# Optimization experiments

Hardware: AMD Instinct MI355X
Metric: run time of the kernel (lower is better)

Reference implementation:

```python
import jax, jax.numpy as jnp
import numpy as np

HID, HQ, HKV, D, W = 2880, 64, 8, 64, 128  # hidden, q heads, kv heads, head_dim, sliding window
SCALE = D ** -0.5
NEG = -1e30


def _rope(x, cos, sin):
    # x: [B,S,H,D]; cos/sin: [S, D//2]
    c = cos[None, :, None, :].astype(x.dtype)
    s = sin[None, :, None, :].astype(x.dtype)
    x1, x2 = jnp.split(x, 2, axis=-1)
    return jnp.concatenate([x1 * c - x2 * s, x2 * c + x1 * s], axis=-1)


def setup_inputs() -> dict:
    key = jax.random.key(0)
    ks = jax.random.split(key, 12)
    B, S = 1, 4096
    std = 0.02
    x = jax.random.normal(ks[0], (B, S, HID), jnp.float32)
    # realistic rotary table (cos || sin), half-dim each
    inv_freq = 1.0 / (150000.0 ** (np.arange(0, D, 2, dtype=np.float32) / D))
    ang = np.arange(S, dtype=np.float32)[:, None] * inv_freq[None, :]
    freqs_cis = jnp.asarray(np.concatenate([np.cos(ang), np.sin(ang)], axis=-1), jnp.float32)  # [S, D]
    Wq = jax.random.normal(ks[1], (HID, HQ * D), jnp.float32) * std
    bq = jnp.zeros((HQ * D,), jnp.float32)
    Wk = jax.random.normal(ks[2], (HID, HKV * D), jnp.float32) * std
    bk = jnp.zeros((HKV * D,), jnp.float32)
    Wv = jax.random.normal(ks[3], (HID, HKV * D), jnp.float32) * std
    bv = jnp.zeros((HKV * D,), jnp.float32)
    Wo = jax.random.normal(ks[4], (HQ * D, HID), jnp.float32) * std
    bo = jnp.zeros((HID,), jnp.float32)
    sinks = jax.random.normal(ks[5], (HQ,), jnp.float32) * std
    return {"x": x, "freqs_cis": freqs_cis, "Wq": Wq, "bq": bq, "Wk": Wk, "bk": bk,
            "Wv": Wv, "bv": bv, "Wo": Wo, "bo": bo, "sinks": sinks}


def reference(x, freqs_cis, Wq, bq, Wk, bk, Wv, bv, Wo, bo, sinks):
    B, S, _ = x.shape
    G = HQ // HKV
    nb = S // W  # S must be a multiple of W
    cos, sin = jnp.split(freqs_cis, 2, axis=-1)

    q = (x @ Wq + bq).reshape(B, S, HQ, D)
    k = (x @ Wk + bk).reshape(B, S, HKV, D)
    v = (x @ Wv + bv).reshape(B, S, HKV, D)
    q = _rope(q, cos, sin)
    k = _rope(k, cos, sin)

    q = q.transpose(0, 2, 1, 3)  # [B,HQ,S,D]
    k = k.transpose(0, 2, 1, 3)  # [B,HKV,S,D]
    v = v.transpose(0, 2, 1, 3)

    # blocked sliding-window: each query block of size W sees keys [blk*W - W, blk*W + W)
    qb = q.reshape(B, HKV, G, nb, W, D)
    kp = jnp.pad(k, ((0, 0), (0, 0), (W, 0), (0, 0)))  # prepend W zero keys
    vp = jnp.pad(v, ((0, 0), (0, 0), (W, 0), (0, 0)))
    widx = jnp.arange(nb)[:, None] * W + jnp.arange(2 * W)[None, :]  # [nb, 2W]
    kb = kp[:, :, widx]  # [B,HKV,nb,2W,D]
    vb = vp[:, :, widx]

    scores = jnp.einsum('bkgntd,bkncd->bkgntc', qb, kb) * SCALE  # [B,HKV,G,nb,W,2W]

    t = jnp.arange(W)[:, None]
    j = jnp.arange(2 * W)[None, :]
    band = (j >= t + 1) & (j <= t + W)  # 0 <= qpos - kpos <= W-1
    kpos_ok = (jnp.arange(nb)[:, None] * W - W + jnp.arange(2 * W)[None, :]) >= 0  # [nb,2W]
    mask = band[None, :, :] & kpos_ok[:, None, :]  # [nb,W,2W]
    scores = jnp.where(mask[None, None, None], scores, NEG)

    sink = sinks.reshape(HKV, G)[None, :, :, None, None]  # [1,HKV,G,1,1]
    m = jnp.maximum(scores.max(axis=-1), sink)  # [B,HKV,G,nb,W]
    e = jnp.exp(scores - m[..., None])
    denom = e.sum(axis=-1) + jnp.exp(sink - m)
    p = e / denom[..., None]

    o = jnp.einsum('bkgntc,bkncd->bkgntd', p, vb)  # [B,HKV,G,nb,W,D]
    o = o.reshape(B, HQ, S, D).transpose(0, 2, 1, 3).reshape(B, S, HQ * D)
    return o @ Wo + bo
```

## Files before the change

kernel.cpp:

```cpp
#include <hip/hip_runtime.h>
#include <hip/hip_bf16.h>
#include <stdint.h>


typedef __attribute__((ext_vector_type(8))) short bf16x8;
typedef __attribute__((ext_vector_type(4))) float f32x4;
typedef __attribute__((ext_vector_type(8))) unsigned short ushort8;

#define DEVI static __device__ __forceinline__

DEVI unsigned short f2bf(float f) {
  unsigned x = __float_as_uint(f);
  return (unsigned short)((x + 0x7fffu + ((x >> 16) & 1u)) >> 16);
}
DEVI float bf2f(unsigned short u) { return __uint_as_float(((unsigned)u) << 16); }

DEVI void async16(const void* g, void* l) {
  __builtin_amdgcn_global_load_lds(
      (const __attribute__((address_space(1))) void*)g,
      (__attribute__((address_space(3))) void*)l, 16, 0, 0);
}

__global__ void k_cast_bf16(const float* __restrict__ src,
                            unsigned short* __restrict__ dst, long n) {
  long i = ((long)blockIdx.x * blockDim.x + threadIdx.x) * 4;
  const long stride = (long)gridDim.x * blockDim.x * 4;
  for (; i < n; i += stride) {
    float4 v = *(const float4*)(src + i);
    ushort4 o = make_ushort4(f2bf(v.x), f2bf(v.y), f2bf(v.z), f2bf(v.w));
    *(ushort4*)(dst + i) = o;
  }
}

__global__ void k_transpose_cast(const float* __restrict__ src,
                                 unsigned short* __restrict__ dst,
                                 int R, int C) {
  __shared__ float tile[64][65];
  const int t = threadIdx.x;
  const int r0 = blockIdx.y * 64, c0 = blockIdx.x * 64;
#pragma unroll
  for (int i = 0; i < 16; i++) {
    int r = i * 4 + (t >> 6), c = t & 63;
    float v = 0.f;
    if (c0 + c < C) v = src[(long)(r0 + r) * C + c0 + c];
    tile[r][c] = v;
  }
  __syncthreads();
#pragma unroll
  for (int i = 0; i < 16; i++) {
    int nn = i * 4 + (t >> 6), kk = t & 63;
    dst[(long)(c0 + nn) * R + r0 + kk] = f2bf(tile[kk][nn]);
  }
}

__global__ void k_concat_bias(const float* __restrict__ bq,
                              const float* __restrict__ bk,
                              const float* __restrict__ bv,
                              float* __restrict__ dst) {
  int i = blockIdx.x * 256 + threadIdx.x;
  if (i < 5120)
    dst[i] = (i < 4096) ? bq[i] : ((i < 4608) ? bk[i - 4096] : bv[i - 4608]);
}

template <bool OUT_BF16, bool NMASK>
__global__ __launch_bounds__(256) void k_gemm_bt(
    const unsigned short* __restrict__ A, const unsigned short* __restrict__ Bt,
    const float* __restrict__ bias, void* __restrict__ Cout, int M, int K,
    int ldc, int Nreal) {
  __shared__ unsigned short As[128 * 32];
  __shared__ unsigned short Bs[128 * 32];
  const int tid = threadIdx.x;
  const int w = tid >> 6, l = tid & 63;
  const int wm = w >> 1, wn = w & 1;
  const int lg = l >> 4, ll = l & 15;
  const long m0 = (long)blockIdx.x * 128;
  const long n0 = (long)blockIdx.y * 128;

  f32x4 acc[4][4];
#pragma unroll
  for (int i = 0; i < 4; i++)
#pragma unroll
    for (int j = 0; j < 4; j++) acc[i][j] = (f32x4){0.f, 0.f, 0.f, 0.f};

  const unsigned short* ga = A + (m0 + 32 * w + (l >> 2)) * (long)K + (l & 3) * 8;
  const unsigned short* gb = Bt + (n0 + 32 * w + (l >> 2)) * (long)K + (l & 3) * 8;
  unsigned short* lA = As + 32 * w * 32;
  unsigned short* lB = Bs + 32 * w * 32;

  for (int kt = 0; kt < K; kt += 32) {
    async16(ga + kt, lA);
    async16(ga + kt + 16 * (long)K, lA + 16 * 32);
    async16(gb + kt, lB);
    async16(gb + kt + 16 * (long)K, lB + 16 * 32);
    __syncthreads();
    bf16x8 af[4], bfr[4];
#pragma unroll
    for (int m = 0; m < 4; m++)
      af[m] = *(const bf16x8*)&As[(wm * 64 + m * 16 + ll) * 32 + 8 * lg];
#pragma unroll
    for (int nn = 0; nn < 4; nn++)
      bfr[nn] = *(const bf16x8*)&Bs[(wn * 64 + nn * 16 + ll) * 32 + 8 * lg];
#pragma unroll
    for (int m = 0; m < 4; m++)
#pragma unroll
      for (int nn = 0; nn < 4; nn++)
        acc[m][nn] = __builtin_amdgcn_mfma_f32_16x16x32_bf16(af[m], bfr[nn],
                                                             acc[m][nn], 0, 0, 0);
    __syncthreads();
  }

#pragma unroll
  for (int nn = 0; nn < 4; nn++) {
    int col = (int)n0 + wn * 64 + nn * 16 + ll;
    bool ok = (!NMASK) || (col < Nreal);
    float bv_ = ok ? bias[col] : 0.f;
#pragma unroll
    for (int m = 0; m < 4; m++) {
      long row = m0 + wm * 64 + m * 16 + lg * 4;
#pragma unroll
      for (int j = 0; j < 4; j++) {
        float v = acc[m][nn][j] + bv_;
        if (ok) {
          if (OUT_BF16)
            ((unsigned short*)Cout)[(row + j) * (long)ldc + col] = f2bf(v);
          else
            ((float*)Cout)[(row + j) * (long)ldc + col] = v;
        }
      }
    }
  }
}

__global__ void k_rope(unsigned short* __restrict__ qkv,
                       const float* __restrict__ fc) {
  const int s = blockIdx.x;
  const float* f = fc + (long)s * 64;
  unsigned short* row = qkv + (long)s * 5120;
  for (int i = threadIdx.x; i < 72 * 32; i += 256) {
    int hh = i >> 5, d = i & 31;
    float c = f[d], sn = f[32 + d];
    int base = hh * 64 + d;
    float x1 = bf2f(row[base]), x2 = bf2f(row[base + 32]);
    row[base] = f2bf(x1 * c - x2 * sn);
    row[base + 32] = f2bf(x2 * c + x1 * sn);
  }
}

__global__ void k_transpose_v(const unsigned short* __restrict__ qkv,
                              unsigned short* __restrict__ vt) {
  __shared__ unsigned short tile[64][72];
  const int t = threadIdx.x;
  const int ts = blockIdx.x;
  const int tj = blockIdx.y;
#pragma unroll
  for (int i = 0; i < 2; i++) {
    int s = i * 32 + (t >> 3), j = (t & 7) * 8;
    *(ushort8*)&tile[s][j] =
        *(const ushort8*)(qkv + (long)(ts * 64 + s) * 5120 + 4608 + tj * 64 + j);
  }
  __syncthreads();
  int j = t >> 2, s0 = (t & 3) * 16;
  ushort8 v0, v1;
#pragma unroll
  for (int x = 0; x < 8; x++) {
    v0[x] = tile[s0 + x][j];
    v1[x] = tile[s0 + 8 + x][j];
  }
  unsigned short* dst = vt + (long)(tj * 64 + j) * 4096 + ts * 64 + s0;
  *(ushort8*)dst = v0;
  *(ushort8*)(dst + 8) = v1;
}

__global__ __launch_bounds__(256) void k_attn(
    const unsigned short* __restrict__ qkv, const unsigned short* __restrict__ vt,
    const float* __restrict__ sinks, unsigned short* __restrict__ o) {
  __shared__ unsigned short Ps[4][32][136];
  __shared__ unsigned short Ks[128][72];
  __shared__ unsigned short Vts[64][136];
  unsigned short(*Qs)[72] = (unsigned short(*)[72]) & Ps[0][0][0];

  const int n = blockIdx.x, h = blockIdx.y;
  const int kvh = h >> 3;
  const int t = threadIdx.x, w = t >> 6, l = t & 63;
  const int lg = l >> 4, ll = l & 15;

#pragma unroll
  for (int i = 0; i < 4; i++) {
    int s = 32 * i + (t >> 3), c8 = (t & 7) * 8;
    *(ushort8*)&Qs[s][c8] =
        *(const ushort8*)(qkv + (long)(n * 128 + s) * 5120 + h * 64 + c8);
  }
  __syncthreads();
  bf16x8 aq[2][2];
#pragma unroll
  for (int m = 0; m < 2; m++)
#pragma unroll
    for (int ks = 0; ks < 2; ks++)
      aq[m][ks] = *(const bf16x8*)&Qs[32 * w + 16 * m + ll][32 * ks + 8 * lg];

  f32x4 oacc[2][4];
#pragma unroll
  for (int m = 0; m < 2; m++)
#pragma unroll
    for (int nt = 0; nt < 4; nt++) oacc[m][nt] = (f32x4){0.f, 0.f, 0.f, 0.f};
  float mrun[2][4], lrun[2][4];
#pragma unroll
  for (int m = 0; m < 2; m++)
#pragma unroll
    for (int j = 0; j < 4; j++) { mrun[m][j] = -3.0e38f; lrun[m][j] = 0.f; }

  for (int ch = (n == 0 ? 1 : 0); ch < 2; ch++) {
    const int kbase = (n - 1 + ch) * 128;
#pragma unroll
    for (int i = 0; i < 4; i++) {
      int c = 32 * i + (t >> 3), c8 = (t & 7) * 8;
      *(ushort8*)&Ks[c][c8] = *(const ushort8*)(
          qkv + (long)(kbase + c) * 5120 + 4096 + kvh * 64 + c8);
    }
#pragma unroll
    for (int i = 0; i < 4; i++) {
      int d = 16 * i + (t >> 4), c8 = (t & 15) * 8;
      *(ushort8*)&Vts[d][c8] =
          *(const ushort8*)(vt + (long)(kvh * 64 + d) * 4096 + kbase + c8);
    }
    __syncthreads();

    f32x4 sacc[2][8];
#pragma unroll
    for (int m = 0; m < 2; m++)
#pragma unroll
      for (int ct = 0; ct < 8; ct++) sacc[m][ct] = (f32x4){0.f, 0.f, 0.f, 0.f};
#pragma unroll
    for (int ct = 0; ct < 8; ct++)
#pragma unroll
      for (int ks = 0; ks < 2; ks++) {
        bf16x8 bk = *(const bf16x8*)&Ks[16 * ct + ll][32 * ks + 8 * lg];
#pragma unroll
        for (int m = 0; m < 2; m++)
          sacc[m][ct] =
              __builtin_amdgcn_mfma_f32_16x16x32_bf16(aq[m][ks], bk, sacc[m][ct], 0, 0, 0);
      }

    float cmax[2][4];
#pragma unroll
    for (int m = 0; m < 2; m++)
#pragma unroll
      for (int j = 0; j < 4; j++) cmax[m][j] = -3.0e38f;
#pragma unroll
    for (int m = 0; m < 2; m++)
#pragma unroll
      for (int ct = 0; ct < 8; ct++)
#pragma unroll
        for (int j = 0; j < 4; j++) {
          int trow = 32 * w + 16 * m + 4 * lg + j;
          int cc = ch * 128 + 16 * ct + ll;
          bool valid = (cc >= trow + 1) && (cc <= trow + 128);
          float sv = valid ? sacc[m][ct][j] * 0.125f : -1.0e30f;
          sacc[m][ct][j] = sv;
          cmax[m][j] = fmaxf(cmax[m][j], sv);
        }
#pragma unroll
    for (int m = 0; m < 2; m++)
#pragma unroll
      for (int j = 0; j < 4; j++) {
        float v = cmax[m][j];
#pragma unroll
        for (int off = 1; off < 16; off <<= 1) v = fmaxf(v, __shfl_xor(v, off));
        cmax[m][j] = v;
      }

    float fsc[2][4];
#pragma unroll
    for (int m = 0; m < 2; m++)
#pragma unroll
      for (int j = 0; j < 4; j++) {
        float mnew = fmaxf(mrun[m][j], cmax[m][j]);
        fsc[m][j] = __expf(mrun[m][j] - mnew);
        mrun[m][j] = mnew;
        lrun[m][j] *= fsc[m][j];
      }

    float psum[2][4];
#pragma unroll
    for (int m = 0; m < 2; m++)
#pragma unroll
      for (int j = 0; j < 4; j++) psum[m][j] = 0.f;
#pragma unroll
    for (int m = 0; m < 2; m++)
#pragma unroll
      for (int ct = 0; ct < 8; ct++)
#pragma unroll
        for (int j = 0; j < 4; j++) {
          float p = __expf(sacc[m][ct][j] - mrun[m][j]);
          psum[m][j] += p;
          Ps[w][16 * m + 4 * lg + j][16 * ct + ll] = f2bf(p);
        }
#pragma unroll
    for (int m = 0; m < 2; m++)
#pragma unroll
      for (int j = 0; j < 4; j++) {
        float v = psum[m][j];
#pragma unroll
        for (int off = 1; off < 16; off <<= 1) v += __shfl_xor(v, off);
        lrun[m][j] += v;
#pragma unroll
        for (int nt = 0; nt < 4; nt++) oacc[m][nt][j] *= fsc[m][j];
      }

    asm volatile("s_waitcnt lgkmcnt(0)" ::: "memory");

#pragma unroll
    for (int ks = 0; ks < 4; ks++) {
      bf16x8 pa[2], vb[4];
#pragma unroll
      for (int m = 0; m < 2; m++)
        pa[m] = *(const bf16x8*)&Ps[w][16 * m + ll][32 * ks + 8 * lg];
#pragma unroll
      for (int nt = 0; nt < 4; nt++)
        vb[nt] = *(const bf16x8*)&Vts[16 * nt + ll][32 * ks + 8 * lg];
#pragma unroll
      for (int m = 0; m < 2; m++)
#pragma unroll
        for (int nt = 0; nt < 4; nt++)
          oacc[m][nt] =
              __builtin_amdgcn_mfma_f32_16x16x32_bf16(pa[m], vb[nt], oacc[m][nt], 0, 0, 0);
    }
    __syncthreads();
  }

  const float sk = sinks[h];
#pragma unroll
  for (int m = 0; m < 2; m++)
#pragma unroll
    for (int j = 0; j < 4; j++) {
      float mf = fmaxf(mrun[m][j], sk);
      float f = __expf(mrun[m][j] - mf);
      float denom = lrun[m][j] * f + __expf(sk - mf);
      float sc = f / denom;
#pragma unroll
      for (int nt = 0; nt < 4; nt++) oacc[m][nt][j] *= sc;
    }
#pragma unroll
  for (int m = 0; m < 2; m++)
#pragma unroll
    for (int nt = 0; nt < 4; nt++)
#pragma unroll
      for (int j = 0; j < 4; j++) {
        long row = (long)n * 128 + 32 * w + 16 * m + 4 * lg + j;
        int col = h * 64 + 16 * nt + ll;
        o[row * 4096 + col] = f2bf(oacc[m][nt][j]);
      }
}

extern "C" void kernel_launch(void* const* d_in, const int* in_sizes, int n_in,
                              void* d_out, int out_size, void* d_ws,
                              size_t ws_size, hipStream_t stream) {
  const float* x = (const float*)d_in[0];
  const float* fc = (const float*)d_in[1];
  const float* Wq = (const float*)d_in[2];
  const float* bq = (const float*)d_in[3];
  const float* Wk = (const float*)d_in[4];
  const float* bk = (const float*)d_in[5];
  const float* Wv = (const float*)d_in[6];
  const float* bv = (const float*)d_in[7];
  const float* Wo = (const float*)d_in[8];
  const float* bo = (const float*)d_in[9];
  const float* sinks = (const float*)d_in[10];
  float* out = (float*)d_out;

  char* p = (char*)d_ws;
  unsigned short* xb = (unsigned short*)p;     p += (size_t)4096 * 2880 * 2;
  unsigned short* Wqkvt = (unsigned short*)p;  p += (size_t)5120 * 2880 * 2;
  unsigned short* Wot = (unsigned short*)p;    p += (size_t)2944 * 4096 * 2;
  unsigned short* qkv = (unsigned short*)p;    p += (size_t)4096 * 5120 * 2;
  unsigned short* vt = (unsigned short*)p;     p += (size_t)512 * 4096 * 2;
  unsigned short* obuf = (unsigned short*)p;   p += (size_t)4096 * 4096 * 2;
  float* biasq = (float*)p;                    p += (size_t)5120 * 4;

  k_cast_bf16<<<2048, 256, 0, stream>>>(x, xb, (long)4096 * 2880);
  k_transpose_cast<<<dim3(64, 45), 256, 0, stream>>>(Wq, Wqkvt, 2880, 4096);
  k_transpose_cast<<<dim3(8, 45), 256, 0, stream>>>(
      Wk, Wqkvt + (size_t)4096 * 2880, 2880, 512);
  k_transpose_cast<<<dim3(8, 45), 256, 0, stream>>>(
      Wv, Wqkvt + (size_t)4608 * 2880, 2880, 512);
  k_transpose_cast<<<dim3(46, 64), 256, 0, stream>>>(Wo, Wot, 4096, 2880);
  k_concat_bias<<<20, 256, 0, stream>>>(bq, bk, bv, biasq);

  k_gemm_bt<true, false><<<dim3(32, 40), 256, 0, stream>>>(
      xb, Wqkvt, biasq, qkv, 4096, 2880, 5120, 5120);

  k_rope<<<4096, 256, 0, stream>>>(qkv, fc);
  k_transpose_v<<<dim3(64, 8), 256, 0, stream>>>(qkv, vt);

  k_attn<<<dim3(32, 64), 256, 0, stream>>>(qkv, vt, sinks, obuf);

  k_gemm_bt<false, true><<<dim3(32, 23), 256, 0, stream>>>(
      obuf, Wot, bo, out, 4096, 4096, 2880, 2880);
}
```

Before: 708.1 us.

## Replace GEMM with 256x256-tile, 8-wave, double-buffered swizzled LDS pipeline

Replaces the 128x128 single-buffered GEMM with a 512-thread kernel that computes 256x256 output tiles. It double-buffers K=64 stages through async global-to-LDS loads, using an XOR swizzle against bank conflicts, and interleaves the loads with MFMA quarters under s_setprio. Blocks are remapped so consecutive tiles land on the same XCD for L2 reuse, and the attention output buffer is aliased onto the cast-x workspace. The aim is higher arithmetic intensity and overlap of memory with MFMA in both projection GEMMs. The cost is fewer blocks (320 and 192) on a 256-CU part, which risks tail imbalance, plus large LDS use per block.

```diff
diff --git a/kernel.cpp b/kernel.cpp
--- a/kernel.cpp
+++ b/kernel.cpp
@@ -62,61 +62,125 @@
     dst[i] = (i < 4096) ? bq[i] : ((i < 4608) ? bk[i - 4096] : bv[i - 4608]);
 }
 
+#define STG(c, half, t)                                                        \
+  do {                                                                         \
+    const int tt_ = ((t) < NT) ? (t) : NT - 1;                                 \
+    const long ko_ = (long)tt_ * 64;                                           \
+    if ((half) < 2) {                                                          \
+      const unsigned short* s_ = gA + (long)(half) * 128 * Kd + ko_;           \
+      unsigned short* d_ = &As_[c][(((half) * 128) + w8) * 64];                \
+      async16(s_, d_);                                                         \
+      async16(s_ + 64 * (long)Kd, d_ + 64 * 64);                               \
+    } else {                                                                   \
+      const unsigned short* s_ = gB + (long)((half) - 2) * 128 * Kd + ko_;     \
+      unsigned short* d_ = &Bs_[c][((((half) - 2) * 128) + w8) * 64];          \
+      async16(s_, d_);                                                         \
+      async16(s_ + 64 * (long)Kd, d_ + 64 * 64);                               \
+    }                                                                          \
+  } while (0)
+
+#define LOADA(c, mh)                                                           \
+  do {                                                                         \
+    _Pragma("unroll") for (int m4 = 0; m4 < 4; m4++) {                         \
+      const unsigned short* r_ =                                               \
+          &As_[c][(wr128 + ((mh)*4 + m4) * 16 + ll) * 64];                     \
+      aF[m4][0] = *(const bf16x8*)(r_ + sl0 * 8);                              \
+      aF[m4][1] = *(const bf16x8*)(r_ + sl1 * 8);                              \
+    }                                                                          \
+  } while (0)
+
+#define LOADB(c, nh)                                                           \
+  do {                                                                         \
+    _Pragma("unroll") for (int n2 = 0; n2 < 2; n2++) {                         \
+      const unsigned short* r_ =                                               \
+          &Bs_[c][(wc64 + ((nh)*2 + n2) * 16 + ll) * 64];                      \
+      bF[nh][n2][0] = *(const bf16x8*)(r_ + sl0 * 8);                          \
+      bF[nh][n2][1] = *(const bf16x8*)(r_ + sl1 * 8);                          \
+    }                                                                          \
+  } while (0)
+
+#define MFMAQ(mh, nh)                                                          \
+  do {                                                                         \
+    __builtin_amdgcn_s_setprio(1);                                             \
+    _Pragma("unroll") for (int m4 = 0; m4 < 4; m4++)                           \
+        _Pragma("unroll") for (int n2 = 0; n2 < 2; n2++) {                     \
+      acc[(mh)*4 + m4][(nh)*2 + n2] = __builtin_amdgcn_mfma_f32_16x16x32_bf16( \
+          aF[m4][0], bF[nh][n2][0], acc[(mh)*4 + m4][(nh)*2 + n2], 0, 0, 0);   \
+      acc[(mh)*4 + m4][(nh)*2 + n2] = __builtin_amdgcn_mfma_f32_16x16x32_bf16( \
+          aF[m4][1], bF[nh][n2][1], acc[(mh)*4 + m4][(nh)*2 + n2], 0, 0, 0);   \
+    }                                                                          \
+    __builtin_amdgcn_s_setprio(0);                                             \
+  } while (0)
+
+#define BAR() __builtin_amdgcn_s_barrier()
+#define VM2() asm volatile("s_waitcnt vmcnt(2)" ::: "memory")
+
 template <bool OUT_BF16, bool NMASK>
-__global__ __launch_bounds__(256) void k_gemm_bt(
+__global__ __launch_bounds__(512, 2) void k_gemm8(
     const unsigned short* __restrict__ A, const unsigned short* __restrict__ Bt,
-    const float* __restrict__ bias, void* __restrict__ Cout, int M, int K,
-    int ldc, int Nreal) {
-  __shared__ unsigned short As[128 * 32];
-  __shared__ unsigned short Bs[128 * 32];
+    const float* __restrict__ bias, void* __restrict__ Cout,
+    int Kd, int NN, int ldc, int Nreal) {
+  __shared__ unsigned short As_[2][256 * 64];
+  __shared__ unsigned short Bs_[2][256 * 64];
   const int tid = threadIdx.x;
   const int w = tid >> 6, l = tid & 63;
-  const int wm = w >> 1, wn = w & 1;
+  const int wr = w >> 2, wc = w & 3;
   const int lg = l >> 4, ll = l & 15;
-  const long m0 = (long)blockIdx.x * 128;
-  const long n0 = (long)blockIdx.y * 128;
-
-  f32x4 acc[4][4];
-#pragma unroll
-  for (int i = 0; i < 4; i++)
+  const int w8 = w * 8;
+  const int wr128 = wr * 128, wc64 = wc * 64;
+  const int sl0 = lg ^ (ll & 7), sl1 = sl0 ^ 4;
+  const int NT = Kd >> 6;
+
+  const int b = blockIdx.x;
+  const int cpx = gridDim.x >> 3;
+  const int tile = (b & 7) * cpx + (b >> 3);
+  const int tm = tile / NN, tn = tile % NN;
+  const long m0 = (long)tm * 256, n0 = (long)tn * 256;
+
+  const unsigned short* gA =
+      A + (m0 + (tid >> 3)) * (long)Kd + (((tid & 7) ^ ((tid >> 3) & 7)) << 3);
+  const unsigned short* gB =
+      Bt + (n0 + (tid >> 3)) * (long)Kd + (((tid & 7) ^ ((tid >> 3) & 7)) << 3);
+
+  f32x4 acc[8][4];
+#pragma unroll
+  for (int i = 0; i < 8; i++)
 #pragma unroll
     for (int j = 0; j < 4; j++) acc[i][j] = (f32x4){0.f, 0.f, 0.f, 0.f};
-
-  const unsigned short* ga = A + (m0 + 32 * w + (l >> 2)) * (long)K + (l & 3) * 8;
-  const unsigned short* gb = Bt + (n0 + 32 * w + (l >> 2)) * (long)K + (l & 3) * 8;
-  unsigned short* lA = As + 32 * w * 32;
-  unsigned short* lB = Bs + 32 * w * 32;
-
-  for (int kt = 0; kt < K; kt += 32) {
-    async16(ga + kt, lA);
-    async16(ga + kt + 16 * (long)K, lA + 16 * 32);
-    async16(gb + kt, lB);
-    async16(gb + kt + 16 * (long)K, lB + 16 * 32);
-    __syncthreads();
-    bf16x8 af[4], bfr[4];
-#pragma unroll
-    for (int m = 0; m < 4; m++)
-      af[m] = *(const bf16x8*)&As[(wm * 64 + m * 16 + ll) * 32 + 8 * lg];
-#pragma unroll
-    for (int nn = 0; nn < 4; nn++)
-      bfr[nn] = *(const bf16x8*)&Bs[(wn * 64 + nn * 16 + ll) * 32 + 8 * lg];
-#pragma unroll
-    for (int m = 0; m < 4; m++)
-#pragma unroll
-      for (int nn = 0; nn < 4; nn++)
-        acc[m][nn] = __builtin_amdgcn_mfma_f32_16x16x32_bf16(af[m], bfr[nn],
-                                                             acc[m][nn], 0, 0, 0);
-    __syncthreads();
+  bf16x8 aF[4][2], bF[2][2][2];
+
+  STG(0, 0, 0); STG(0, 1, 0); STG(0, 2, 0); STG(0, 3, 0);
+  STG(1, 0, 1);
+  VM2();
+  BAR();
+
+  const int NITER = NT >> 1;
+  for (int i = 0; i < NITER; i++) {
+    const int t = 2 * i;
+    LOADA(0, 0); LOADB(0, 0); STG(1, 1, t + 1); BAR(); MFMAQ(0, 0); BAR();
+    LOADB(0, 1);              STG(1, 2, t + 1); BAR(); MFMAQ(0, 1); BAR();
+    LOADA(0, 1);              STG(1, 3, t + 1); BAR(); MFMAQ(1, 1); BAR();
+    STG(0, 0, t + 2); VM2();                    BAR(); MFMAQ(1, 0); BAR();
+    LOADA(1, 0); LOADB(1, 0); STG(0, 1, t + 2); BAR(); MFMAQ(0, 0); BAR();
+    LOADB(1, 1);              STG(0, 2, t + 2); BAR(); MFMAQ(0, 1); BAR();
+    LOADA(1, 1);              STG(0, 3, t + 2); BAR(); MFMAQ(1, 1); BAR();
+    STG(1, 0, t + 3); VM2();                    BAR(); MFMAQ(1, 0); BAR();
+  }
+  if (NT & 1) {
+    LOADA(0, 0); LOADB(0, 0); MFMAQ(0, 0);
+    LOADB(0, 1); MFMAQ(0, 1);
+    LOADA(0, 1); MFMAQ(1, 1);
+    MFMAQ(1, 0);
   }
 
 #pragma unroll
   for (int nn = 0; nn < 4; nn++) {
-    int col = (int)n0 + wn * 64 + nn * 16 + ll;
+    int col = (int)n0 + wc64 + nn * 16 + ll;
     bool ok = (!NMASK) || (col < Nreal);
     float bv_ = ok ? bias[col] : 0.f;
 #pragma unroll
-    for (int m = 0; m < 4; m++) {
-      long row = m0 + wm * 64 + m * 16 + lg * 4;
+    for (int m = 0; m < 8; m++) {
+      long row = m0 + wr128 + m * 16 + lg * 4;
 #pragma unroll
       for (int j = 0; j < 4; j++) {
         float v = acc[m][nn][j] + bv_;
@@ -237,8 +301,8 @@
         bf16x8 bk = *(const bf16x8*)&Ks[16 * ct + ll][32 * ks + 8 * lg];
 #pragma unroll
         for (int m = 0; m < 2; m++)
-          sacc[m][ct] =
-              __builtin_amdgcn_mfma_f32_16x16x32_bf16(aq[m][ks], bk, sacc[m][ct], 0, 0, 0);
+          sacc[m][ct] = __builtin_amdgcn_mfma_f32_16x16x32_bf16(
+              aq[m][ks], bk, sacc[m][ct], 0, 0, 0);
       }
 
     float cmax[2][4];
@@ -322,8 +386,8 @@
       for (int m = 0; m < 2; m++)
 #pragma unroll
         for (int nt = 0; nt < 4; nt++)
-          oacc[m][nt] =
-              __builtin_amdgcn_mfma_f32_16x16x32_bf16(pa[m], vb[nt], oacc[m][nt], 0, 0, 0);
+          oacc[m][nt] = __builtin_amdgcn_mfma_f32_16x16x32_bf16(
+              pa[m], vb[nt], oacc[m][nt], 0, 0, 0);
     }
     __syncthreads();
   }
@@ -369,12 +433,13 @@
   float* out = (float*)d_out;
 
   char* p = (char*)d_ws;
-  unsigned short* xb = (unsigned short*)p;     p += (size_t)4096 * 2880 * 2;
+  unsigned short* xb = (unsigned short*)p;
+  unsigned short* obuf = (unsigned short*)p;
+  p += (size_t)4096 * 2880 * 2;
   unsigned short* Wqkvt = (unsigned short*)p;  p += (size_t)5120 * 2880 * 2;
-  unsigned short* Wot = (unsigned short*)p;    p += (size_t)2944 * 4096 * 2;
+  unsigned short* Wot = (unsigned short*)p;    p += (size_t)3072 * 4096 * 2;
   unsigned short* qkv = (unsigned short*)p;    p += (size_t)4096 * 5120 * 2;
   unsigned short* vt = (unsigned short*)p;     p += (size_t)512 * 4096 * 2;
-  unsigned short* obuf = (unsigned short*)p;   p += (size_t)4096 * 4096 * 2;
   float* biasq = (float*)p;                    p += (size_t)5120 * 4;
 
   k_cast_bf16<<<2048, 256, 0, stream>>>(x, xb, (long)4096 * 2880);
@@ -383,17 +448,17 @@
       Wk, Wqkvt + (size_t)4096 * 2880, 2880, 512);
   k_transpose_cast<<<dim3(8, 45), 256, 0, stream>>>(
       Wv, Wqkvt + (size_t)4608 * 2880, 2880, 512);
-  k_transpose_cast<<<dim3(46, 64), 256, 0, stream>>>(Wo, Wot, 4096, 2880);
+  k_transpose_cast<<<dim3(48, 64), 256, 0, stream>>>(Wo, Wot, 4096, 2880);
   k_concat_bias<<<20, 256, 0, stream>>>(bq, bk, bv, biasq);
 
-  k_gemm_bt<true, false><<<dim3(32, 40), 256, 0, stream>>>(
-      xb, Wqkvt, biasq, qkv, 4096, 2880, 5120, 5120);
+  k_gemm8<true, false><<<16 * 20, 512, 0, stream>>>(
+      xb, Wqkvt, biasq, qkv, 2880, 20, 5120, 5120);
 
   k_rope<<<4096, 256, 0, stream>>>(qkv, fc);
   k_transpose_v<<<dim3(64, 8), 256, 0, stream>>>(qkv, vt);
 
   k_attn<<<dim3(32, 64), 256, 0, stream>>>(qkv, vt, sinks, obuf);
 
-  k_gemm_bt<false, true><<<dim3(32, 23), 256, 0, stream>>>(
-      obuf, Wot, bo, out, 4096, 4096, 2880, 2880);
-}
+  k_gemm8<false, true><<<16 * 12, 512, 0, stream>>>(
+      obuf, Wot, bo, out, 4096, 12, 2880, 2880);
+}
```

New measurement: 654.7 us. 7.5% less time.
